# Optimization experiments

Hardware: AMD Instinct MI355X
Metric: run time of the kernel (lower is better)

The kernel has to match this reference:

```python
import jax, jax.numpy as jnp
import numpy as np


def _parallel_scan_affine(log_a, b):
    """Hillis-Steele doubling scan for h_t = a_t*h_{t-1} + b_t (h_0 = 0).

    log_a, b: (B, T, d). Operator: (la2,b2) o (la1,b1) = (la1+la2, exp(la2)*b1 + b2).
    """
    T = log_a.shape[1]
    la, bv = log_a, b
    stride = 1
    while stride < T:  # static Python loop, log2(T) rounds
        la_prev = jnp.roll(la, stride, axis=1).at[:, :stride, :].set(0.0)
        bv_prev = jnp.roll(bv, stride, axis=1).at[:, :stride, :].set(0.0)
        bv = jnp.exp(la) * bv_prev + bv
        la = la + la_prev
        stride *= 2
    return bv


def setup_inputs() -> dict:
    key = jax.random.key(0)
    kx, kwz, kwh = jax.random.split(key, 3)
    B, T, D = 4, 4096, 1024
    x = jax.random.normal(kx, (B, T, D), dtype=jnp.float32)
    # nn.Linear(D, D) weights, stored as (out, in) like torch
    Wz = jax.random.normal(kwz, (D, D), dtype=jnp.float32) * 0.02
    bz = jnp.zeros((D,), dtype=jnp.float32)
    Wh = jax.random.normal(kwh, (D, D), dtype=jnp.float32) * 0.02
    bh = jnp.zeros((D,), dtype=jnp.float32)
    return {"x": x, "Wz": Wz, "bz": bz, "Wh": Wh, "bh": bh}


def reference(x, Wz, bz, Wh, bh):
    # forward_parallel: z = sigmoid(linear_z(x)); h_tilde = linear_h(x)
    z = jax.nn.sigmoid(jnp.einsum("btd,ed->bte", x, Wz) + bz)
    h_tilde = jnp.einsum("btd,ed->bte", x, Wh) + bh
    log_a = jnp.log(1.0 - z + 1e-08)
    b = z * h_tilde
    h_out = _parallel_scan_affine(log_a, b)
    return h_out  # out_proj is Identity since d_inner == d_model
```

## Files before the change

### kernel.cpp

```cpp
#include <hip/hip_runtime.h>
#include <hip/hip_bf16.h>


typedef __bf16 bf16x8 __attribute__((ext_vector_type(8)));
typedef __bf16 bf16x4 __attribute__((ext_vector_type(4)));
typedef float  f32x4  __attribute__((ext_vector_type(4)));

#define BSZ 4
#define TSZ 4096
#define DSZ 1024
#define MSZ (BSZ*TSZ)
#define CH  32
#define NC  (TSZ/CH)

__device__ __forceinline__ void gload_lds16(const __bf16* g, __bf16* l) {
  __builtin_amdgcn_global_load_lds(
      (const __attribute__((address_space(1))) void*)g,
      (__attribute__((address_space(3))) void*)l, 16, 0, 0);
}

__global__ void convert_tile_kernel(const float* __restrict__ X,
                                    const float* __restrict__ Wz,
                                    const float* __restrict__ Wh,
                                    __bf16* __restrict__ Xc,
                                    __bf16* __restrict__ Wzc,
                                    __bf16* __restrict__ Whc)
{
  const int bx = blockIdx.x;
  const float* src; __bf16* dst; int gid;
  if (bx < 8192)      { src = X;  dst = Xc;  gid =  bx        *256 + threadIdx.x; }
  else if (bx < 8704) { src = Wz; dst = Wzc; gid = (bx - 8192)*256 + threadIdx.x; }
  else                { src = Wh; dst = Whc; gid = (bx - 8704)*256 + threadIdx.x; }
  const int l    = gid & 63;
  const int i    = (gid >> 6) & 7;
  const int kblk = (gid >> 9) & 31;
  const int rblk = gid >> 14;
  const int row  = rblk*128 + i*16 + (l & 15);
  const int col  = kblk*32 + (l >> 4)*8;
  const float* g = src + (size_t)row*DSZ + col;
  float4 v0 = *(const float4*)g;
  float4 v1 = *(const float4*)(g + 4);
  bf16x8 p;
  p[0]=(__bf16)v0.x; p[1]=(__bf16)v0.y; p[2]=(__bf16)v0.z; p[3]=(__bf16)v0.w;
  p[4]=(__bf16)v1.x; p[5]=(__bf16)v1.y; p[6]=(__bf16)v1.z; p[7]=(__bf16)v1.w;
  *(bf16x8*)(dst + (size_t)gid*8) = p;
}

__global__ __launch_bounds__(256, 2) void gemm_gate_kernel(
    const __bf16* __restrict__ Xc,  const __bf16* __restrict__ Wzc,
    const __bf16* __restrict__ Whc,
    const float* __restrict__ bz, const float* __restrict__ bh,
    __bf16* __restrict__ a_ws, float* __restrict__ b_out,
    float* __restrict__ Aprod, float* __restrict__ Bcomp)
{
  __shared__ __align__(16) __bf16 As [4096];
  __shared__ __align__(16) __bf16 Bzs[4096];
  __shared__ __align__(16) __bf16 Bhs[4096];

  const int tid  = threadIdx.x;
  const int lane = tid & 63;
  const int wv   = tid >> 6;
  const int wM   = (wv >> 1) * 64;
  const int wN   = (wv & 1) * 64;
  const int wMg  = wM >> 4;
  const int wNg  = wN >> 4;
  const int lr   = lane & 15;
  const int q    = lane >> 4;
  const int wbase = wv * 64;

  const __bf16* Xb = Xc  + (size_t)blockIdx.x * 32 * 4096;
  const __bf16* Zb = Wzc + (size_t)blockIdx.y * 32 * 4096;
  const __bf16* Hb = Whc + (size_t)blockIdx.y * 32 * 4096;

  f32x4 accz[4][4] = {};
  f32x4 acch[4][4] = {};

  for (int kblk = 0; kblk < 32; ++kblk) {
    __syncthreads();
    const size_t tb = (size_t)kblk * 4096;
    #pragma unroll
    for (int c = 0; c < 2; ++c) {
      const int eo = (c*256 + wbase + lane) * 8;
      const int lo = (c*256 + wbase) * 8;
      gload_lds16(Xb + tb + eo, As  + lo);
      gload_lds16(Zb + tb + eo, Bzs + lo);
      gload_lds16(Hb + tb + eo, Bhs + lo);
    }
    __syncthreads();

    bf16x8 af[4];
    #pragma unroll
    for (int i = 0; i < 4; ++i)
      af[i] = *(const bf16x8*)(As + (wMg + i)*512 + lane*8);
    #pragma unroll
    for (int j = 0; j < 4; ++j) {
      bf16x8 bz8 = *(const bf16x8*)(Bzs + (wNg + j)*512 + lane*8);
      bf16x8 bh8 = *(const bf16x8*)(Bhs + (wNg + j)*512 + lane*8);
      #pragma unroll
      for (int i = 0; i < 4; ++i) {
        accz[j][i] = __builtin_amdgcn_mfma_f32_16x16x32_bf16(af[i], bz8, accz[j][i], 0, 0, 0);
        acch[j][i] = __builtin_amdgcn_mfma_f32_16x16x32_bf16(af[i], bh8, acch[j][i], 0, 0, 0);
      }
    }
  }

  const int M0 = blockIdx.x * 128;
  const int N0 = blockIdx.y * 128;
  #pragma unroll
  for (int j = 0; j < 4; ++j) {
    const int e = N0 + wN + j*16 + lr;
    const float bzv = bz[e];
    const float bhv = bh[e];
    float Aseg[4], Bseg[4];
    #pragma unroll
    for (int i = 0; i < 4; ++i) {
      const int mbase = M0 + wM + i*16 + q*4;
      float A = 1.0f, Bv = 0.0f;
      #pragma unroll
      for (int r = 0; r < 4; ++r) {
        const size_t idx = (size_t)(mbase + r)*DSZ + e;
        const float pz = accz[j][i][r] + bzv;
        const float ph = acch[j][i][r] + bhv;
        const float ex = __expf(-pz);
        const float z  = 1.0f / (1.0f + ex);
        const __bf16 abf = (__bf16)fmaf(ex, z, 1e-8f);
        const float  af  = (float)abf;
        const float  bf  = z * ph;
        a_ws[idx]  = abf;
        b_out[idx] = bf;
        Bv = fmaf(af, Bv, bf);
        A *= af;
      }
      Aseg[i] = A; Bseg[i] = Bv;
    }
    #pragma unroll
    for (int i = 0; i < 4; ++i) {
      #pragma unroll
      for (int s = 16; s < 64; s <<= 1) {
        const float Ap = __shfl_up(Aseg[i], s, 64);
        const float Bp = __shfl_up(Bseg[i], s, 64);
        if (lane >= s) { Bseg[i] = fmaf(Aseg[i], Bp, Bseg[i]); Aseg[i] *= Ap; }
      }
    }
    if (q == 3) {
      #pragma unroll
      for (int c = 0; c < 2; ++c) {
        const float Ac = Aseg[2*c+1] * Aseg[2*c];
        const float Bc = fmaf(Aseg[2*c+1], Bseg[2*c], Bseg[2*c+1]);
        const int bc = (M0 + wM + c*32) >> 5;
        Aprod[(size_t)bc*DSZ + e] = Ac;
        Bcomp[(size_t)bc*DSZ + e] = Bc;
      }
    }
  }
}

__global__ void scan_pass2_kernel(const float* __restrict__ Aprod,
                                  const float* __restrict__ Bcomp,
                                  float* __restrict__ Hstart)
{
  const int lane = threadIdx.x & 63;
  const int wave = (blockIdx.x * 256 + threadIdx.x) >> 6;
  const int b = wave >> 10;
  const int d = wave & 1023;
  const size_t i0 = (size_t)(b*NC + 2*lane)*DSZ + d;
  const float A0 = Aprod[i0],       B0 = Bcomp[i0];
  const float A1 = Aprod[i0 + DSZ], B1 = Bcomp[i0 + DSZ];
  float A  = A0 * A1;
  float Bv = fmaf(A1, B0, B1);
  #pragma unroll
  for (int s = 1; s < 64; s <<= 1) {
    const float Ap = __shfl_up(A,  s, 64);
    const float Bp = __shfl_up(Bv, s, 64);
    if (lane >= s) { Bv = fmaf(A, Bp, Bv); A *= Ap; }
  }
  float Hp = __shfl_up(Bv, 1, 64);
  if (lane == 0) Hp = 0.0f;
  Hstart[i0]       = Hp;
  Hstart[i0 + DSZ] = fmaf(A0, Hp, B0);
}

__global__ void scan_pass3_kernel(const __bf16* __restrict__ a_ws,
                                  const float* __restrict__ Hstart,
                                  float* __restrict__ out)
{
  const int bc   = blockIdx.x;
  const int d0   = threadIdx.x * 4;
  const size_t base = (size_t)bc * CH * DSZ + d0;
  float4 hv = *(const float4*)(Hstart + (size_t)bc*DSZ + d0);
  float h[4] = {hv.x, hv.y, hv.z, hv.w};
  #pragma unroll 8
  for (int t = 0; t < CH; ++t) {
    bf16x4 a4 = *(const bf16x4*)(a_ws + base + (size_t)t*DSZ);
    float4 b4 = *(const float4*)(out + base + (size_t)t*DSZ);
    const float bb[4] = {b4.x, b4.y, b4.z, b4.w};
    #pragma unroll
    for (int c = 0; c < 4; ++c)
      h[c] = fmaf((float)a4[c], h[c], bb[c]);
    *(float4*)(out + base + (size_t)t*DSZ) = make_float4(h[0], h[1], h[2], h[3]);
  }
}

extern "C" void kernel_launch(void* const* d_in, const int* in_sizes, int n_in,
                              void* d_out, int out_size, void* d_ws, size_t ws_size,
                              hipStream_t stream)
{
  const float* x  = (const float*)d_in[0];
  const float* Wz = (const float*)d_in[1];
  const float* bz = (const float*)d_in[2];
  const float* Wh = (const float*)d_in[3];
  const float* bh = (const float*)d_in[4];
  float* out = (float*)d_out;

  __bf16* Xc   = (__bf16*)d_ws;
  __bf16* Wzc  = Xc  + (size_t)MSZ * DSZ;
  __bf16* Whc  = Wzc + (size_t)DSZ * DSZ;
  __bf16* a_ws = Whc + (size_t)DSZ * DSZ;
  float* Aprod  = (float*)(a_ws + (size_t)MSZ * DSZ);
  float* Bcomp  = Aprod + (size_t)BSZ*NC*DSZ;
  float* Hstart = Bcomp + (size_t)BSZ*NC*DSZ;

  convert_tile_kernel<<<9216, 256, 0, stream>>>(x, Wz, Wh, Xc, Wzc, Whc);
  gemm_gate_kernel<<<dim3(MSZ/128, DSZ/128), 256, 0, stream>>>(
      Xc, Wzc, Whc, bz, bh, a_ws, out, Aprod, Bcomp);
  scan_pass2_kernel<<<(BSZ*DSZ)/4, 256, 0, stream>>>(Aprod, Bcomp, Hstart);
  scan_pass3_kernel<<<BSZ*NC, 256, 0, stream>>>(a_ws, Hstart, out);
}
```

Before: 242.2 us.

## Double GEMM K-tile per barrier and halve scan chunk length

The GEMM now stages two 32-wide K slices per barrier pair, using 48KB of LDS instead of 24KB and half as many k-iterations and syncs. The scan chunk shrinks from 32 to 16 timesteps: the GEMM epilogue writes per-16-row segment summaries directly, pass2 combines four chunks per lane, and pass3 fully unrolls a shorter serial loop with twice as many blocks. Hstart reuses the Aprod buffer in place, which is why restrict was dropped there. The larger LDS footprint may reduce occupancy, and pass2 now handles twice the summary data.

```diff
diff --git a/kernel.cpp b/kernel.cpp
--- a/kernel.cpp
+++ b/kernel.cpp
@@ -10,7 +10,7 @@
 #define TSZ 4096
 #define DSZ 1024
 #define MSZ (BSZ*TSZ)
-#define CH  32
+#define CH  16
 #define NC  (TSZ/CH)
 
 __device__ __forceinline__ void gload_lds16(const __bf16* g, __bf16* l) {
@@ -53,9 +53,9 @@
     __bf16* __restrict__ a_ws, float* __restrict__ b_out,
     float* __restrict__ Aprod, float* __restrict__ Bcomp)
 {
-  __shared__ __align__(16) __bf16 As [4096];
-  __shared__ __align__(16) __bf16 Bzs[4096];
-  __shared__ __align__(16) __bf16 Bhs[4096];
+  __shared__ __align__(16) __bf16 As [8192];
+  __shared__ __align__(16) __bf16 Bzs[8192];
+  __shared__ __align__(16) __bf16 Bhs[8192];
 
   const int tid  = threadIdx.x;
   const int lane = tid & 63;
@@ -75,11 +75,11 @@
   f32x4 accz[4][4] = {};
   f32x4 acch[4][4] = {};
 
-  for (int kblk = 0; kblk < 32; ++kblk) {
+  for (int kblk = 0; kblk < 16; ++kblk) {
     __syncthreads();
-    const size_t tb = (size_t)kblk * 4096;
-    #pragma unroll
-    for (int c = 0; c < 2; ++c) {
+    const size_t tb = (size_t)kblk * 8192;
+    #pragma unroll
+    for (int c = 0; c < 4; ++c) {
       const int eo = (c*256 + wbase + lane) * 8;
       const int lo = (c*256 + wbase) * 8;
       gload_lds16(Xb + tb + eo, As  + lo);
@@ -88,18 +88,22 @@
     }
     __syncthreads();
 
-    bf16x8 af[4];
-    #pragma unroll
-    for (int i = 0; i < 4; ++i)
-      af[i] = *(const bf16x8*)(As + (wMg + i)*512 + lane*8);
-    #pragma unroll
-    for (int j = 0; j < 4; ++j) {
-      bf16x8 bz8 = *(const bf16x8*)(Bzs + (wNg + j)*512 + lane*8);
-      bf16x8 bh8 = *(const bf16x8*)(Bhs + (wNg + j)*512 + lane*8);
-      #pragma unroll
-      for (int i = 0; i < 4; ++i) {
-        accz[j][i] = __builtin_amdgcn_mfma_f32_16x16x32_bf16(af[i], bz8, accz[j][i], 0, 0, 0);
-        acch[j][i] = __builtin_amdgcn_mfma_f32_16x16x32_bf16(af[i], bh8, acch[j][i], 0, 0, 0);
+    #pragma unroll
+    for (int h = 0; h < 2; ++h) {
+      const int ho = h * 4096;
+      bf16x8 af[4];
+      #pragma unroll
+      for (int i = 0; i < 4; ++i)
+        af[i] = *(const bf16x8*)(As + ho + (wMg + i)*512 + lane*8);
+      #pragma unroll
+      for (int j = 0; j < 4; ++j) {
+        bf16x8 bz8 = *(const bf16x8*)(Bzs + ho + (wNg + j)*512 + lane*8);
+        bf16x8 bh8 = *(const bf16x8*)(Bhs + ho + (wNg + j)*512 + lane*8);
+        #pragma unroll
+        for (int i = 0; i < 4; ++i) {
+          accz[j][i] = __builtin_amdgcn_mfma_f32_16x16x32_bf16(af[i], bz8, accz[j][i], 0, 0, 0);
+          acch[j][i] = __builtin_amdgcn_mfma_f32_16x16x32_bf16(af[i], bh8, acch[j][i], 0, 0, 0);
+        }
       }
     }
   }
@@ -144,40 +148,46 @@
     }
     if (q == 3) {
       #pragma unroll
-      for (int c = 0; c < 2; ++c) {
-        const float Ac = Aseg[2*c+1] * Aseg[2*c];
-        const float Bc = fmaf(Aseg[2*c+1], Bseg[2*c], Bseg[2*c+1]);
-        const int bc = (M0 + wM + c*32) >> 5;
-        Aprod[(size_t)bc*DSZ + e] = Ac;
-        Bcomp[(size_t)bc*DSZ + e] = Bc;
-      }
-    }
-  }
-}
-
-__global__ void scan_pass2_kernel(const float* __restrict__ Aprod,
+      for (int i = 0; i < 4; ++i) {
+        const int bc = (M0 + wM + i*16) >> 4;
+        Aprod[(size_t)bc*DSZ + e] = Aseg[i];
+        Bcomp[(size_t)bc*DSZ + e] = Bseg[i];
+      }
+    }
+  }
+}
+
+__global__ void scan_pass2_kernel(const float* Aprod,
                                   const float* __restrict__ Bcomp,
-                                  float* __restrict__ Hstart)
+                                  float* Hstart)
 {
   const int lane = threadIdx.x & 63;
   const int wave = (blockIdx.x * 256 + threadIdx.x) >> 6;
   const int b = wave >> 10;
   const int d = wave & 1023;
-  const size_t i0 = (size_t)(b*NC + 2*lane)*DSZ + d;
-  const float A0 = Aprod[i0],       B0 = Bcomp[i0];
-  const float A1 = Aprod[i0 + DSZ], B1 = Bcomp[i0 + DSZ];
-  float A  = A0 * A1;
-  float Bv = fmaf(A1, B0, B1);
+  const size_t i0 = (size_t)(b*NC + 4*lane)*DSZ + d;
+  float Ac[4], Bc[4];
+  #pragma unroll
+  for (int c = 0; c < 4; ++c) {
+    Ac[c] = Aprod[i0 + (size_t)c*DSZ];
+    Bc[c] = Bcomp[i0 + (size_t)c*DSZ];
+  }
+  float A = Ac[0], Bv = Bc[0];
+  #pragma unroll
+  for (int c = 1; c < 4; ++c) { Bv = fmaf(Ac[c], Bv, Bc[c]); A *= Ac[c]; }
   #pragma unroll
   for (int s = 1; s < 64; s <<= 1) {
     const float Ap = __shfl_up(A,  s, 64);
     const float Bp = __shfl_up(Bv, s, 64);
     if (lane >= s) { Bv = fmaf(A, Bp, Bv); A *= Ap; }
   }
-  float Hp = __shfl_up(Bv, 1, 64);
-  if (lane == 0) Hp = 0.0f;
-  Hstart[i0]       = Hp;
-  Hstart[i0 + DSZ] = fmaf(A0, Hp, B0);
+  float h = __shfl_up(Bv, 1, 64);
+  if (lane == 0) h = 0.0f;
+  #pragma unroll
+  for (int c = 0; c < 4; ++c) {
+    Hstart[i0 + (size_t)c*DSZ] = h;
+    h = fmaf(Ac[c], h, Bc[c]);
+  }
 }
 
 __global__ void scan_pass3_kernel(const __bf16* __restrict__ a_ws,
@@ -189,7 +199,7 @@
   const size_t base = (size_t)bc * CH * DSZ + d0;
   float4 hv = *(const float4*)(Hstart + (size_t)bc*DSZ + d0);
   float h[4] = {hv.x, hv.y, hv.z, hv.w};
-  #pragma unroll 8
+  #pragma unroll
   for (int t = 0; t < CH; ++t) {
     bf16x4 a4 = *(const bf16x4*)(a_ws + base + (size_t)t*DSZ);
     float4 b4 = *(const float4*)(out + base + (size_t)t*DSZ);
@@ -218,7 +228,7 @@
   __bf16* a_ws = Whc + (size_t)DSZ * DSZ;
   float* Aprod  = (float*)(a_ws + (size_t)MSZ * DSZ);
   float* Bcomp  = Aprod + (size_t)BSZ*NC*DSZ;
-  float* Hstart = Bcomp + (size_t)BSZ*NC*DSZ;
+  float* Hstart = Aprod;
 
   convert_tile_kernel<<<9216, 256, 0, stream>>>(x, Wz, Wh, Xc, Wzc, Whc);
   gemm_gate_kernel<<<dim3(MSZ/128, DSZ/128), 256, 0, stream>>>(
```

New measurement: 256.3 us. +5.8%, slower.
